# Kernel optimization log

Measured on AMD Instinct MI355X. Metric: run time of the kernel, lower is better.

## Reference

```python
import jax, jax.numpy as jnp
import numpy as np

FEATURE_DIM, HIDDEN_DIM, ATTN_DIM = 2048, 1024, 1024
B, L = 128, 196


def setup_inputs() -> dict:
    key = jax.random.key(0)
    ks = jax.random.split(key, 8)
    s_enc = 1.0 / np.sqrt(FEATURE_DIM)
    s_hid = 1.0 / np.sqrt(HIDDEN_DIM)
    s_full = 1.0 / np.sqrt(ATTN_DIM)
    return {
        "encoder_out": jax.random.normal(ks[0], (B, L, FEATURE_DIM), jnp.float32),
        "hidden": jax.random.normal(ks[1], (B, HIDDEN_DIM), jnp.float32),
        "W_enc": jax.random.uniform(ks[2], (FEATURE_DIM, ATTN_DIM), jnp.float32, -s_enc, s_enc),
        "b_enc": jax.random.uniform(ks[3], (ATTN_DIM,), jnp.float32, -s_enc, s_enc),
        "W_hid": jax.random.uniform(ks[4], (HIDDEN_DIM, ATTN_DIM), jnp.float32, -s_hid, s_hid),
        "b_hid": jax.random.uniform(ks[5], (ATTN_DIM,), jnp.float32, -s_hid, s_hid),
        "W_full": jax.random.uniform(ks[6], (ATTN_DIM,), jnp.float32, -s_full, s_full),
        "b_full": jax.random.uniform(ks[7], (1,), jnp.float32, -s_full, s_full),
    }


def reference(encoder_out, hidden, W_enc, b_enc, W_hid, b_hid, W_full, b_full):
    # attn1: (B, L, A)
    attn1 = jnp.einsum("blf,fa->bla", encoder_out, W_enc) + b_enc
    # attn2: (B, 1, A)
    attn2 = (hidden @ W_hid + b_hid)[:, None, :]
    attn = jax.nn.relu(attn1 + attn2)
    # scalar score per location: (B, L)
    scores = jnp.einsum("bla,a->bl", attn, W_full) + b_full[0]
    alpha = jax.nn.softmax(scores, axis=1)
    # weighted sum over L: (B, F)
    context = jnp.einsum("blf,bl->bf", encoder_out, alpha)
    return context, alpha
```

## Files before the change

### kernel.cpp

```cpp
#include <hip/hip_runtime.h>
#include <hip/hip_bf16.h>

typedef unsigned short u16;
typedef short s16x8 __attribute__((ext_vector_type(8)));
typedef float f32x4 __attribute__((ext_vector_type(4)));

#define F_DIM 2048
#define A_DIM 1024
#define H_DIM 1024
#define BATCH 128
#define LLEN  196
#define MROWS (BATCH * LLEN)
#define LDA   40

__device__ __forceinline__ u16 f2b(float x) {
  union { float f; unsigned int u; } c; c.f = x;
  unsigned int r = (c.u + 0x7fffu + ((c.u >> 16) & 1u)) >> 16;
  return (u16)r;
}

__global__ void wenc_cvt_kernel(const float* __restrict__ W, u16* __restrict__ WT) {
  __shared__ float tile[32][33];
  int kb = blockIdx.x * 32, ab = blockIdx.y * 32;
  int t = threadIdx.x;
  int r = t >> 3, c = (t & 7) * 4;
  float4 v = *(const float4*)&W[(size_t)(kb + r) * A_DIM + ab + c];
  tile[r][c] = v.x; tile[r][c + 1] = v.y; tile[r][c + 2] = v.z; tile[r][c + 3] = v.w;
  __syncthreads();
  ushort4 o;
  o.x = f2b(tile[c + 0][r]);
  o.y = f2b(tile[c + 1][r]);
  o.z = f2b(tile[c + 2][r]);
  o.w = f2b(tile[c + 3][r]);
  *(ushort4*)&WT[(size_t)(ab + r) * F_DIM + kb + c] = o;
}

__global__ void attn2_kernel(const float* __restrict__ hidden, const float* __restrict__ W_hid,
                             const float* __restrict__ b_hid, const float* __restrict__ b_enc,
                             float* __restrict__ attn2p) {
  __shared__ float hl[8][256];
  int t = threadIdx.x;
  int a  = blockIdx.x * 256 + t;
  int b0 = blockIdx.y * 8;
  int k0 = blockIdx.z * 256;
  {
    int j = t >> 5, kk = (t & 31) * 8;
    float4 v0 = *(const float4*)&hidden[(size_t)(b0 + j) * H_DIM + k0 + kk];
    float4 v1 = *(const float4*)&hidden[(size_t)(b0 + j) * H_DIM + k0 + kk + 4];
    hl[j][kk + 0] = v0.x; hl[j][kk + 1] = v0.y; hl[j][kk + 2] = v0.z; hl[j][kk + 3] = v0.w;
    hl[j][kk + 4] = v1.x; hl[j][kk + 5] = v1.y; hl[j][kk + 6] = v1.z; hl[j][kk + 7] = v1.w;
  }
  __syncthreads();
  float acc[8] = {0.f, 0.f, 0.f, 0.f, 0.f, 0.f, 0.f, 0.f};
  #pragma unroll 4
  for (int k = 0; k < 256; ++k) {
    float w = W_hid[(size_t)(k0 + k) * A_DIM + a];
    #pragma unroll
    for (int j = 0; j < 8; ++j) acc[j] = fmaf(hl[j][k], w, acc[j]);
  }
  if (blockIdx.z == 0) {
    float bias = b_hid[a] + b_enc[a];
    #pragma unroll
    for (int j = 0; j < 8; ++j) acc[j] += bias;
  }
  #pragma unroll
  for (int j = 0; j < 8; ++j) atomicAdd(&attn2p[(size_t)(b0 + j) * A_DIM + a], acc[j]);
}

__global__ void gemm_score_kernel(const float* __restrict__ enc, const u16* __restrict__ WT,
                                  const float* __restrict__ attn2p, const float* __restrict__ W_full,
                                  float* __restrict__ scores) {
  __shared__ __align__(16) u16 As[128 * LDA];
  __shared__ __align__(16) u16 Bs[128 * LDA];
  __shared__ float wf_lds[128];
  __shared__ float at2_lds[2][128];

  int n0 = blockIdx.x * 128;
  int m0 = blockIdx.y * 128;
  int t = threadIdx.x;

  int b0 = m0 / LLEN;
  int bnd = (b0 + 1) * LLEN;
  int b1 = min(b0 + 1, BATCH - 1);

  if (t < 128) {
    wf_lds[t] = W_full[n0 + t];
    at2_lds[0][t] = attn2p[(size_t)b0 * A_DIM + n0 + t];
    at2_lds[1][t] = attn2p[(size_t)b1 * A_DIM + n0 + t];
  }

  int lane = t & 63, wave = t >> 6;
  int wr = wave >> 1, wc = wave & 1;
  int c16 = lane & 15, quad = lane >> 4;

  f32x4 acc[4][4];
  #pragma unroll
  for (int i = 0; i < 4; ++i)
    #pragma unroll
    for (int j = 0; j < 4; ++j) acc[i][j] = (f32x4){0.f, 0.f, 0.f, 0.f};

  int ar = t >> 3, ac = (t & 7) * 4;
  int br = t >> 2, bc = (t & 3) * 8;
  const float* ap = enc + (size_t)(m0 + ar) * F_DIM + ac;
  const u16*  bp = WT + (size_t)(n0 + br) * F_DIM + bc;

  for (int kt = 0; kt < F_DIM; kt += 32) {
    #pragma unroll
    for (int p = 0; p < 4; ++p) {
      float4 v = *(const float4*)(ap + (size_t)p * 32 * F_DIM + kt);
      ushort4 u;
      u.x = f2b(v.x); u.y = f2b(v.y); u.z = f2b(v.z); u.w = f2b(v.w);
      *(ushort4*)&As[(ar + p * 32) * LDA + ac] = u;
    }
    #pragma unroll
    for (int p = 0; p < 2; ++p) {
      uint4 v = *(const uint4*)(bp + (size_t)p * 64 * F_DIM + kt);
      *(uint4*)&Bs[(br + p * 64) * LDA + bc] = v;
    }
    __syncthreads();
    s16x8 af[4], bf[4];
    #pragma unroll
    for (int i = 0; i < 4; ++i) {
      af[i] = *(const s16x8*)&As[(wr * 64 + i * 16 + c16) * LDA + quad * 8];
      bf[i] = *(const s16x8*)&Bs[(wc * 64 + i * 16 + c16) * LDA + quad * 8];
    }
    #pragma unroll
    for (int mi = 0; mi < 4; ++mi)
      #pragma unroll
      for (int ni = 0; ni < 4; ++ni)
        acc[mi][ni] = __builtin_amdgcn_mfma_f32_16x16x32_bf16(af[mi], bf[ni], acc[mi][ni], 0, 0, 0);
    __syncthreads();
  }

  float wf[4], a2a[4], a2b[4];
  #pragma unroll
  for (int ni = 0; ni < 4; ++ni) {
    int col = wc * 64 + ni * 16 + c16;
    wf[ni] = wf_lds[col];
    a2a[ni] = at2_lds[0][col];
    a2b[ni] = at2_lds[1][col];
  }
  #pragma unroll
  for (int mi = 0; mi < 4; ++mi) {
    #pragma unroll
    for (int r = 0; r < 4; ++r) {
      int row_g = m0 + wr * 64 + mi * 16 + quad * 4 + r;
      bool hi = row_g >= bnd;
      float p = 0.f;
      #pragma unroll
      for (int ni = 0; ni < 4; ++ni) {
        float v = acc[mi][ni][r] + (hi ? a2b[ni] : a2a[ni]);
        v = fmaxf(v, 0.f);
        p = fmaf(v, wf[ni], p);
      }
      p += __shfl_xor(p, 1);
      p += __shfl_xor(p, 2);
      p += __shfl_xor(p, 4);
      p += __shfl_xor(p, 8);
      if (c16 == 0) atomicAdd(&scores[row_g], p);
    }
  }
}

__global__ void softmax_kernel(const float* __restrict__ scores, float* __restrict__ alpha) {
  __shared__ float red[8];
  int b = blockIdx.x, t = threadIdx.x;
  float s = (t < LLEN) ? scores[b * LLEN + t] : -3.0e38f;
  float m = s;
  #pragma unroll
  for (int o = 1; o <= 32; o <<= 1) m = fmaxf(m, __shfl_xor(m, o));
  if ((t & 63) == 0) red[t >> 6] = m;
  __syncthreads();
  m = fmaxf(fmaxf(red[0], red[1]), fmaxf(red[2], red[3]));
  float e = (t < LLEN) ? expf(s - m) : 0.f;
  float sum = e;
  #pragma unroll
  for (int o = 1; o <= 32; o <<= 1) sum += __shfl_xor(sum, o);
  __syncthreads();
  if ((t & 63) == 0) red[4 + (t >> 6)] = sum;
  __syncthreads();
  sum = red[4] + red[5] + red[6] + red[7];
  if (t < LLEN) alpha[b * LLEN + t] = e / sum;
}

__global__ void context_kernel(const float* __restrict__ enc, const float* __restrict__ alpha,
                               float* __restrict__ out) {
  __shared__ float al[LLEN];
  int b = blockIdx.y, t = threadIdx.x;
  int f4 = blockIdx.x * 256 + t;
  if (t < LLEN) al[t] = alpha[b * LLEN + t];
  __syncthreads();
  const float4* e4 = (const float4*)enc + (size_t)b * LLEN * (F_DIM / 4) + f4;
  float4 acc = {0.f, 0.f, 0.f, 0.f};
  #pragma unroll 4
  for (int l = 0; l < LLEN; ++l) {
    float4 v = e4[(size_t)l * (F_DIM / 4)];
    float a = al[l];
    acc.x = fmaf(v.x, a, acc.x);
    acc.y = fmaf(v.y, a, acc.y);
    acc.z = fmaf(v.z, a, acc.z);
    acc.w = fmaf(v.w, a, acc.w);
  }
  ((float4*)out)[(size_t)b * (F_DIM / 4) + f4] = acc;
}

extern "C" void kernel_launch(void* const* d_in, const int* in_sizes, int n_in,
                              void* d_out, int out_size, void* d_ws, size_t ws_size,
                              hipStream_t stream) {
  const float* enc    = (const float*)d_in[0];
  const float* hidden = (const float*)d_in[1];
  const float* W_enc  = (const float*)d_in[2];
  const float* b_enc  = (const float*)d_in[3];
  const float* W_hid  = (const float*)d_in[4];
  const float* b_hid  = (const float*)d_in[5];
  const float* W_full = (const float*)d_in[6];
  float* out = (float*)d_out;

  char* ws = (char*)d_ws;
  u16*   WT     = (u16*)ws;
  float* attn2p = (float*)(ws + (size_t)A_DIM * F_DIM * sizeof(u16));
  float* scores = (float*)(ws + (size_t)A_DIM * F_DIM * sizeof(u16) + (size_t)BATCH * A_DIM * sizeof(float));

  hipMemsetAsync(attn2p, 0, (size_t)BATCH * A_DIM * sizeof(float), stream);
  hipMemsetAsync(scores, 0, (size_t)MROWS * sizeof(float), stream);

  float* alpha_out = out + (size_t)BATCH * F_DIM;

  wenc_cvt_kernel<<<dim3(F_DIM / 32, A_DIM / 32), 256, 0, stream>>>(W_enc, WT);
  attn2_kernel<<<dim3(A_DIM / 256, BATCH / 8, 4), 256, 0, stream>>>(hidden, W_hid, b_hid, b_enc, attn2p);
  gemm_score_kernel<<<dim3(A_DIM / 128, MROWS / 128), 256, 0, stream>>>(enc, WT, attn2p, W_full, scores);
  softmax_kernel<<<dim3(BATCH), 256, 0, stream>>>(scores, alpha_out);
  context_kernel<<<dim3(F_DIM / 4 / 256, BATCH), 256, 0, stream>>>(enc, alpha_out, out);
}
```

Baseline: 575.3 us.

## Use direct global-to-LDS loads with swizzle, grouped tile order, split context and attn2

The GEMM now loads fp32 encoder rows and bf16 weight rows straight into LDS with global_load_lds and an XOR swizzle, then converts A to bf16 with packed cvt instructions at fragment-read time. Thread blocks are remapped so groups of 8 M-tiles share N-tiles, which should improve L2 reuse of the encoder data. The context reduction is split four ways over L with atomic accumulation into a zeroed output, and attn2 is split over more K chunks. These changes target global load latency, register staging and low occupancy, but they double the fp32 A tile in LDS and add atomics and an extra memset.

```diff
diff --git a/kernel.cpp b/kernel.cpp
--- a/kernel.cpp
+++ b/kernel.cpp
@@ -3,6 +3,7 @@
 
 typedef unsigned short u16;
 typedef short s16x8 __attribute__((ext_vector_type(8)));
+typedef unsigned int u32x4 __attribute__((ext_vector_type(4)));
 typedef float f32x4 __attribute__((ext_vector_type(4)));
 
 #define F_DIM 2048
@@ -11,12 +12,22 @@
 #define BATCH 128
 #define LLEN  196
 #define MROWS (BATCH * LLEN)
-#define LDA   40
 
 __device__ __forceinline__ u16 f2b(float x) {
   union { float f; unsigned int u; } c; c.f = x;
   unsigned int r = (c.u + 0x7fffu + ((c.u >> 16) & 1u)) >> 16;
   return (u16)r;
+}
+
+__device__ __forceinline__ unsigned int f2b_pk(float a, float b) {
+  unsigned int r;
+  asm volatile("v_cvt_pk_bf16_f32 %0, %1, %2" : "=v"(r) : "v"(a), "v"(b));
+  return r;
+}
+
+__device__ __forceinline__ void gload_lds16(const void* g, void* l) {
+  __builtin_amdgcn_global_load_lds((const __attribute__((address_space(1))) void*)g,
+                                   (__attribute__((address_space(3))) void*)l, 16, 0, 0);
 }
 
 __global__ void wenc_cvt_kernel(const float* __restrict__ W, u16* __restrict__ WT) {
@@ -38,22 +49,20 @@
 __global__ void attn2_kernel(const float* __restrict__ hidden, const float* __restrict__ W_hid,
                              const float* __restrict__ b_hid, const float* __restrict__ b_enc,
                              float* __restrict__ attn2p) {
-  __shared__ float hl[8][256];
+  __shared__ float hl[8][128];
   int t = threadIdx.x;
   int a  = blockIdx.x * 256 + t;
   int b0 = blockIdx.y * 8;
-  int k0 = blockIdx.z * 256;
+  int k0 = blockIdx.z * 128;
   {
-    int j = t >> 5, kk = (t & 31) * 8;
-    float4 v0 = *(const float4*)&hidden[(size_t)(b0 + j) * H_DIM + k0 + kk];
-    float4 v1 = *(const float4*)&hidden[(size_t)(b0 + j) * H_DIM + k0 + kk + 4];
-    hl[j][kk + 0] = v0.x; hl[j][kk + 1] = v0.y; hl[j][kk + 2] = v0.z; hl[j][kk + 3] = v0.w;
-    hl[j][kk + 4] = v1.x; hl[j][kk + 5] = v1.y; hl[j][kk + 6] = v1.z; hl[j][kk + 7] = v1.w;
+    int j = t >> 5, kk = (t & 31) * 4;
+    float4 v = *(const float4*)&hidden[(size_t)(b0 + j) * H_DIM + k0 + kk];
+    hl[j][kk + 0] = v.x; hl[j][kk + 1] = v.y; hl[j][kk + 2] = v.z; hl[j][kk + 3] = v.w;
   }
   __syncthreads();
   float acc[8] = {0.f, 0.f, 0.f, 0.f, 0.f, 0.f, 0.f, 0.f};
   #pragma unroll 4
-  for (int k = 0; k < 256; ++k) {
+  for (int k = 0; k < 128; ++k) {
     float w = W_hid[(size_t)(k0 + k) * A_DIM + a];
     #pragma unroll
     for (int j = 0; j < 8; ++j) acc[j] = fmaf(hl[j][k], w, acc[j]);
@@ -67,16 +76,24 @@
   for (int j = 0; j < 8; ++j) atomicAdd(&attn2p[(size_t)(b0 + j) * A_DIM + a], acc[j]);
 }
 
-__global__ void gemm_score_kernel(const float* __restrict__ enc, const u16* __restrict__ WT,
-                                  const float* __restrict__ attn2p, const float* __restrict__ W_full,
-                                  float* __restrict__ scores) {
-  __shared__ __align__(16) u16 As[128 * LDA];
-  __shared__ __align__(16) u16 Bs[128 * LDA];
+__global__ void gemm_score(const float* __restrict__ enc, const u16* __restrict__ WT,
+                           const float* __restrict__ attn2p, const float* __restrict__ W_full,
+                           float* __restrict__ scores) {
+  __shared__ __align__(16) float Asf[128 * 32];
+  __shared__ __align__(16) u16 Bs[128 * 32];
   __shared__ float wf_lds[128];
   __shared__ float at2_lds[2][128];
 
-  int n0 = blockIdx.x * 128;
-  int m0 = blockIdx.y * 128;
+  int i = blockIdx.x;
+  int g  = i >> 6;
+  int r  = i & 63;
+  int y  = r >> 3;
+  int gi = r & 7;
+  int mt = g * 8 + gi;
+  if (mt >= MROWS / 128) return;
+
+  int n0 = y * 128;
+  int m0 = mt * 128;
   int t = threadIdx.x;
 
   int b0 = m0 / LLEN;
@@ -95,34 +112,40 @@
 
   f32x4 acc[4][4];
   #pragma unroll
-  for (int i = 0; i < 4; ++i)
-    #pragma unroll
-    for (int j = 0; j < 4; ++j) acc[i][j] = (f32x4){0.f, 0.f, 0.f, 0.f};
-
-  int ar = t >> 3, ac = (t & 7) * 4;
-  int br = t >> 2, bc = (t & 3) * 8;
-  const float* ap = enc + (size_t)(m0 + ar) * F_DIM + ac;
-  const u16*  bp = WT + (size_t)(n0 + br) * F_DIM + bc;
+  for (int ii = 0; ii < 4; ++ii)
+    #pragma unroll
+    for (int j = 0; j < 4; ++j) acc[ii][j] = (f32x4){0.f, 0.f, 0.f, 0.f};
+
+  const float* agp = enc + (size_t)(m0 + wave * 32 + (lane >> 3)) * F_DIM
+                         + ((lane & 7) ^ ((lane >> 3) & 7)) * 4;
+  float* al = Asf + wave * 1024;
+  const u16* bgp = WT + (size_t)(n0 + (t >> 2)) * F_DIM + ((t & 3) ^ ((t >> 3) & 3)) * 8;
+  u16* bl = Bs + wave * 512;
+
+  int akey = c16 & 7;
+  int bkey = (c16 >> 1) & 3;
 
   for (int kt = 0; kt < F_DIM; kt += 32) {
-    #pragma unroll
-    for (int p = 0; p < 4; ++p) {
-      float4 v = *(const float4*)(ap + (size_t)p * 32 * F_DIM + kt);
-      ushort4 u;
-      u.x = f2b(v.x); u.y = f2b(v.y); u.z = f2b(v.z); u.w = f2b(v.w);
-      *(ushort4*)&As[(ar + p * 32) * LDA + ac] = u;
-    }
-    #pragma unroll
-    for (int p = 0; p < 2; ++p) {
-      uint4 v = *(const uint4*)(bp + (size_t)p * 64 * F_DIM + kt);
-      *(uint4*)&Bs[(br + p * 64) * LDA + bc] = v;
-    }
+    gload_lds16(agp + kt, al);
+    gload_lds16(agp + (size_t)8 * F_DIM + kt, al + 256);
+    gload_lds16(agp + (size_t)16 * F_DIM + kt, al + 512);
+    gload_lds16(agp + (size_t)24 * F_DIM + kt, al + 768);
+    gload_lds16(bgp + kt, bl);
+    gload_lds16(bgp + (size_t)64 * F_DIM + kt, bl + 2048);
     __syncthreads();
     s16x8 af[4], bf[4];
     #pragma unroll
-    for (int i = 0; i < 4; ++i) {
-      af[i] = *(const s16x8*)&As[(wr * 64 + i * 16 + c16) * LDA + quad * 8];
-      bf[i] = *(const s16x8*)&Bs[(wc * 64 + i * 16 + c16) * LDA + quad * 8];
+    for (int ii = 0; ii < 4; ++ii) {
+      int arow = (wr * 64 + ii * 16 + c16) * 32;
+      float4 lo = *(const float4*)&Asf[arow + ((2 * quad) ^ akey) * 4];
+      float4 hi = *(const float4*)&Asf[arow + ((2 * quad + 1) ^ akey) * 4];
+      u32x4 w;
+      w.x = f2b_pk(lo.x, lo.y);
+      w.y = f2b_pk(lo.z, lo.w);
+      w.z = f2b_pk(hi.x, hi.y);
+      w.w = f2b_pk(hi.z, hi.w);
+      af[ii] = __builtin_bit_cast(s16x8, w);
+      bf[ii] = *(const s16x8*)&Bs[(wc * 64 + ii * 16 + c16) * 32 + (quad ^ bkey) * 8];
     }
     #pragma unroll
     for (int mi = 0; mi < 4; ++mi)
@@ -143,13 +166,13 @@
   #pragma unroll
   for (int mi = 0; mi < 4; ++mi) {
     #pragma unroll
-    for (int r = 0; r < 4; ++r) {
-      int row_g = m0 + wr * 64 + mi * 16 + quad * 4 + r;
+    for (int rr = 0; rr < 4; ++rr) {
+      int row_g = m0 + wr * 64 + mi * 16 + quad * 4 + rr;
       bool hi = row_g >= bnd;
       float p = 0.f;
       #pragma unroll
       for (int ni = 0; ni < 4; ++ni) {
-        float v = acc[mi][ni][r] + (hi ? a2b[ni] : a2a[ni]);
+        float v = acc[mi][ni][rr] + (hi ? a2b[ni] : a2a[ni]);
         v = fmaxf(v, 0.f);
         p = fmaf(v, wf[ni], p);
       }
@@ -185,15 +208,16 @@
 
 __global__ void context_kernel(const float* __restrict__ enc, const float* __restrict__ alpha,
                                float* __restrict__ out) {
-  __shared__ float al[LLEN];
+  __shared__ float al[49];
   int b = blockIdx.y, t = threadIdx.x;
+  int l0 = blockIdx.z * 49;
   int f4 = blockIdx.x * 256 + t;
-  if (t < LLEN) al[t] = alpha[b * LLEN + t];
-  __syncthreads();
-  const float4* e4 = (const float4*)enc + (size_t)b * LLEN * (F_DIM / 4) + f4;
+  if (t < 49) al[t] = alpha[b * LLEN + l0 + t];
+  __syncthreads();
+  const float4* e4 = (const float4*)enc + ((size_t)b * LLEN + l0) * (F_DIM / 4) + f4;
   float4 acc = {0.f, 0.f, 0.f, 0.f};
-  #pragma unroll 4
-  for (int l = 0; l < LLEN; ++l) {
+  #pragma unroll 7
+  for (int l = 0; l < 49; ++l) {
     float4 v = e4[(size_t)l * (F_DIM / 4)];
     float a = al[l];
     acc.x = fmaf(v.x, a, acc.x);
@@ -201,7 +225,11 @@
     acc.z = fmaf(v.z, a, acc.z);
     acc.w = fmaf(v.w, a, acc.w);
   }
-  ((float4*)out)[(size_t)b * (F_DIM / 4) + f4] = acc;
+  float* o = out + (size_t)b * F_DIM + f4 * 4;
+  atomicAdd(o + 0, acc.x);
+  atomicAdd(o + 1, acc.y);
+  atomicAdd(o + 2, acc.z);
+  atomicAdd(o + 3, acc.w);
 }
 
 extern "C" void kernel_launch(void* const* d_in, const int* in_sizes, int n_in,
@@ -215,20 +243,23 @@
   const float* b_hid  = (const float*)d_in[5];
   const float* W_full = (const float*)d_in[6];
   float* out = (float*)d_out;
-
+  float* alpha_out = out + (size_t)BATCH * F_DIM;
+
+  const size_t wt_bytes = (size_t)A_DIM * F_DIM * sizeof(u16);
+  const size_t a2_bytes = (size_t)BATCH * A_DIM * sizeof(float);
+  const size_t sc_bytes = (size_t)MROWS * sizeof(float);
   char* ws = (char*)d_ws;
   u16*   WT     = (u16*)ws;
-  float* attn2p = (float*)(ws + (size_t)A_DIM * F_DIM * sizeof(u16));
-  float* scores = (float*)(ws + (size_t)A_DIM * F_DIM * sizeof(u16) + (size_t)BATCH * A_DIM * sizeof(float));
-
-  hipMemsetAsync(attn2p, 0, (size_t)BATCH * A_DIM * sizeof(float), stream);
-  hipMemsetAsync(scores, 0, (size_t)MROWS * sizeof(float), stream);
-
-  float* alpha_out = out + (size_t)BATCH * F_DIM;
+  float* attn2p = (float*)(ws + wt_bytes);
+  float* scores = (float*)(ws + wt_bytes + a2_bytes);
+
+  hipMemsetAsync(attn2p, 0, a2_bytes, stream);
+  hipMemsetAsync(scores, 0, sc_bytes, stream);
+  hipMemsetAsync(out, 0, (size_t)BATCH * F_DIM * sizeof(float), stream);
 
   wenc_cvt_kernel<<<dim3(F_DIM / 32, A_DIM / 32), 256, 0, stream>>>(W_enc, WT);
-  attn2_kernel<<<dim3(A_DIM / 256, BATCH / 8, 4), 256, 0, stream>>>(hidden, W_hid, b_hid, b_enc, attn2p);
-  gemm_score_kernel<<<dim3(A_DIM / 128, MROWS / 128), 256, 0, stream>>>(enc, WT, attn2p, W_full, scores);
+  attn2_kernel<<<dim3(A_DIM / 256, BATCH / 8, H_DIM / 128), 256, 0, stream>>>(hidden, W_hid, b_hid, b_enc, attn2p);
+  gemm_score<<<dim3(1600), 256, 0, stream>>>(enc, WT, attn2p, W_full, scores);
   softmax_kernel<<<dim3(BATCH), 256, 0, stream>>>(scores, alpha_out);
-  context_kernel<<<dim3(F_DIM / 4 / 256, BATCH), 256, 0, stream>>>(enc, alpha_out, out);
-}
+  context_kernel<<<dim3(2, BATCH, 4), 256, 0, stream>>>(enc, alpha_out, out);
+}
```

Result: faster. 500.2 us (-13.1%).
